# Performance work log

Hardware: AMD Instinct MI355X
Metric: run time of the kernel (lower is better)

The kernel has to match this reference:

```python
import jax, jax.numpy as jnp
import numpy as np
from jax import lax

B, N, D, H, K = 4096, 25, 256, 8, 3  # batch*frames, nodes, d_model, heads, conv kernel


def _layernorm(x, g, b, eps=1e-5):
    mu = jnp.mean(x, axis=-1, keepdims=True)
    var = jnp.var(x, axis=-1, keepdims=True)
    return (x - mu) * lax.rsqrt(var + eps) * g + b


def _conv1d(x_bdn, w):
    # x_bdn: [B, D, N], w: [D_out, D_in, K], padding=K//2 (same as torch Conv1d)
    return lax.conv_general_dilated(x_bdn, w, window_strides=(1,),
                                    padding=[(K // 2, K // 2)],
                                    dimension_numbers=('NCH', 'OIH', 'NCH'))


def setup_inputs() -> dict:
    key = jax.random.key(0)
    ks = jax.random.split(key, 12)
    x = jax.random.normal(ks[0], (B, N, D), dtype=jnp.float32)
    # symmetric adjacency with self-loops (skeleton graph surrogate)
    a = jax.random.bernoulli(ks[1], 0.3, (N, N))
    adj = a | a.T | jnp.eye(N, dtype=bool)
    cs = 1.0 / np.sqrt(D * K)
    wq = jax.random.normal(ks[2], (D, D, K), dtype=jnp.float32) * cs
    wk = jax.random.normal(ks[3], (D, D, K), dtype=jnp.float32) * cs
    wv = jax.random.normal(ks[4], (D, D, K), dtype=jnp.float32) * cs
    gq = jnp.ones((D,), jnp.float32); bq = jnp.zeros((D,), jnp.float32)
    gk = jnp.ones((D,), jnp.float32); bk = jnp.zeros((D,), jnp.float32)
    gv = jnp.ones((D,), jnp.float32); bv = jnp.zeros((D,), jnp.float32)
    rel_table = jax.random.normal(ks[5], (2 * N - 1, H), dtype=jnp.float32) * 0.02
    local_bias = jnp.zeros((H, N, N), jnp.float32)
    wo = jax.random.normal(ks[6], (D, D), dtype=jnp.float32) * (1.0 / np.sqrt(D))
    bo = jnp.zeros((D,), jnp.float32)
    return dict(x=x, adj=adj, wq=wq, wk=wk, wv=wv, gq=gq, bq=bq, gk=gk, bk=bk,
                gv=gv, bv=bv, rel_table=rel_table, local_bias=local_bias, wo=wo, bo=bo)


def reference(x, adj, wq, wk, wv, gq, bq, gk, bk, gv, bv, rel_table, local_bias, wo, bo):
    b, n, d = x.shape
    h = local_bias.shape[0]
    dk = d // h
    xp = x.transpose(0, 2, 1)  # [B, D, N]
    # conv QKV projection over node axis + per-projection LayerNorm + residual
    q = x + _layernorm(_conv1d(xp, wq).transpose(0, 2, 1), gq, bq)
    k = x + _layernorm(_conv1d(xp, wk).transpose(0, 2, 1), gk, bk)
    v = x + _layernorm(_conv1d(xp, wv).transpose(0, 2, 1), gv, bv)
    qh = q.reshape(b, n, h, dk).transpose(0, 2, 1, 3)  # [B, H, N, dk]
    kh = k.reshape(b, n, h, dk).transpose(0, 2, 1, 3)
    vh = v.reshape(b, n, h, dk).transpose(0, 2, 1, 3)
    scores = jnp.einsum('bhnd,bhmd->bhnm', qh, kh) / np.sqrt(dk)
    # relative positional bias over node indices
    coords = jnp.arange(n)
    idx = coords[:, None] - coords[None, :] + n - 1  # [N, N]
    rel = rel_table[idx].transpose(2, 0, 1)  # [H, N, N]
    scores = scores + rel[None] + local_bias[None]
    # adjacency mask (local attention): non-neighbors -> -inf
    scores = jnp.where(adj[None, None], scores, jnp.finfo(scores.dtype).min)
    attn = jax.nn.softmax(scores, axis=-1)
    out = jnp.einsum('bhnm,bhmd->bhnd', attn, vh)  # [B, H, N, dk]
    out = out.transpose(0, 2, 1, 3).reshape(b, n, d)
    return out @ wo.T + bo
```

## Files before the change

kernel.cpp:

```cpp
#include <hip/hip_runtime.h>

#define BB 4096
#define NN 25
#define DD 256
#define HH 8
#define DKH 32
#define MM (BB*NN)

typedef __bf16 bf16;
typedef bf16 bf16x8 __attribute__((ext_vector_type(8)));
typedef bf16 bf16x4 __attribute__((ext_vector_type(4)));
typedef float f32x4 __attribute__((ext_vector_type(4)));
typedef _Float16 h16;
typedef h16 h16x2 __attribute__((ext_vector_type(2)));
typedef h16 h16x4 __attribute__((ext_vector_type(4)));
typedef h16 h16x8 __attribute__((ext_vector_type(8)));

__device__ __forceinline__ void async_load16(const void* g, void* l) {
  __builtin_amdgcn_global_load_lds(
      (const __attribute__((address_space(1))) unsigned int*)g,
      (__attribute__((address_space(3))) unsigned int*)l, 16, 0, 0);
}

#define SCHED_FENCE() __builtin_amdgcn_sched_barrier(0)
#define BARRIER() do { SCHED_FENCE(); __builtin_amdgcn_s_barrier(); SCHED_FENCE(); } while (0)
#define WAIT_LGKM0() do { asm volatile("s_waitcnt lgkmcnt(0)" ::: "memory"); SCHED_FENCE(); } while (0)

__global__ __launch_bounds__(256) void k_prep_xpad(const float* __restrict__ x,
                                                   bf16* __restrict__ xpad) {
  int idx = (blockIdx.x * 256 + threadIdx.x) * 8;
  const int total = BB * 27 * 256;
  if (idx >= total) return;
  int b = idx / (27 * 256);
  int rem = idx - b * 27 * 256;
  int j = rem >> 8;
  int d = rem & 255;
  bf16x8 o;
  if (j >= 1 && j <= 25) {
    const float* src = x + ((b * 25 + (j - 1)) * 256 + d);
    #pragma unroll
    for (int t = 0; t < 8; ++t) o[t] = (bf16)src[t];
  } else {
    #pragma unroll
    for (int t = 0; t < 8; ++t) o[t] = (bf16)0.0f;
  }
  *(bf16x8*)(xpad + idx) = o;
}

__global__ __launch_bounds__(256) void k_prep_misc(
    const float* __restrict__ wq, const float* __restrict__ wk, const float* __restrict__ wv,
    const float* __restrict__ rel, const float* __restrict__ lb, const float* __restrict__ wo,
    const void* __restrict__ adj_raw,
    bf16* __restrict__ Wt, bf16* __restrict__ woB, float* __restrict__ mb) {
  const int NWT = 768 * 768;
  const int NWO = 256 * 256;
  const int NMB = HH * NN * 32;
  const int total = NWT + NWO + NMB;
  for (int i = blockIdx.x * blockDim.x + threadIdx.x; i < total; i += gridDim.x * blockDim.x) {
    if (i < NWT) {
      int j = i / 768, kk = i - j * 768;
      int proj = j >> 8, jo = j & 255;
      int tap = kk >> 8, di = kk & 255;
      const float* w = (proj == 0) ? wq : ((proj == 1) ? wk : wv);
      Wt[i] = (bf16)w[(jo * 256 + di) * 3 + tap];
    } else if (i < NWT + NWO) {
      int t = i - NWT;
      woB[t] = (bf16)wo[t];
    } else {
      int t = i - NWT - NWO;
      int pair = t >> 5;
      int m = t & 31;
      int h = pair / 25, ii = pair - h * 25;
      float v = -1e30f;
      if (m < 25) {
        const unsigned char* bytes = (const unsigned char*)adj_raw;
        bool u8 = false;
        for (int s = 0; s < 625; ++s) {
          if ((s & 3) && bytes[s]) { u8 = true; break; }
        }
        int amask = u8 ? (bytes[ii * 25 + m] ? 1 : 0)
                       : (((const int*)adj_raw)[ii * 25 + m] ? 1 : 0);
        if (amask)
          v = rel[(ii - m + 24) * HH + h] + lb[h * 625 + ii * 25 + m];
      }
      mb[t] = v;
    }
  }
}

__global__ __launch_bounds__(512, 2) void k_qkv_gemm8(const bf16* __restrict__ xpad,
                                                      const bf16* __restrict__ Wt,
                                                      bf16* __restrict__ conv) {
  __shared__ bf16 Ab[2][256 * 64];
  __shared__ bf16 Bb[2][256 * 64];

  const int L = blockIdx.x;
  const int sw = (L & 7) * 150 + (L >> 3);
  const int n0 = (sw % 3) * 256;
  const int m0 = (sw / 3) * 256;

  const int tid = threadIdx.x;
  const int lane = tid & 63, wave = tid >> 6;
  const int t16 = lane & 15, quad = lane >> 4;
  const int wr = wave >> 2, wc = wave & 3;

  const int srow = tid >> 3;
  const int sc = ((tid & 7) << 4) ^ ((srow & 7) << 4);
  int aOff[4], bOff[4];
  #pragma unroll
  for (int q = 0; q < 4; ++q) {
    int row = q * 64 + srow;
    int gm = m0 + row;
    int b = gm / 25;
    int n = gm - b * 25;
    aOff[q] = (b * 27 + n) * 512 + sc;
    bOff[q] = (n0 + row) * 1536 + sc;
  }

  const int axr = (t16 & 7) << 3;
  int aoffs[2], boffs[2];
  #pragma unroll
  for (int kk = 0; kk < 2; ++kk) {
    aoffs[kk] = (wr * 128 + t16) * 64 + ((kk * 32 + quad * 8) ^ axr);
    boffs[kk] = (wc * 64 + t16) * 64 + ((kk * 32 + quad * 8) ^ axr);
  }

  f32x4 acc[8][4];
  #pragma unroll
  for (int i = 0; i < 8; ++i)
    #pragma unroll
    for (int j = 0; j < 4; ++j) acc[i][j] = (f32x4){0.f, 0.f, 0.f, 0.f};

  #pragma unroll
  for (int tt = 0; tt < 2; ++tt) {
    char* lb = (char*)&Bb[tt][0] + wave * 1024;
    char* la = (char*)&Ab[tt][0] + wave * 1024;
    #pragma unroll
    for (int q = 0; q < 4; ++q)
      async_load16((const char*)Wt + bOff[q] + tt * 128, lb + q * 8192);
    #pragma unroll
    for (int q = 0; q < 4; ++q)
      async_load16((const char*)xpad + aOff[q] + tt * 128, la + q * 8192);
  }
  asm volatile("s_waitcnt vmcnt(8)" ::: "memory");
  SCHED_FENCE();
  BARRIER();

  for (int u = 0; u < 12; ++u) {
    const int buf = u & 1;
    const bf16* Ac = &Ab[buf][0];
    const bf16* Bc = &Bb[buf][0];
    const int st = u + 2;

    bf16x8 aF[8], bF[8];

    #pragma unroll
    for (int i = 0; i < 4; ++i)
      #pragma unroll
      for (int kk = 0; kk < 2; ++kk)
        aF[i * 2 + kk] = *(const bf16x8*)(Ac + aoffs[kk] + i * 1024);
    #pragma unroll
    for (int j = 0; j < 2; ++j)
      #pragma unroll
      for (int kk = 0; kk < 2; ++kk)
        bF[j * 2 + kk] = *(const bf16x8*)(Bc + boffs[kk] + j * 1024);
    BARRIER();
    WAIT_LGKM0();
    __builtin_amdgcn_s_setprio(1);
    #pragma unroll
    for (int i = 0; i < 4; ++i)
      #pragma unroll
      for (int j = 0; j < 2; ++j)
        #pragma unroll
        for (int kk = 0; kk < 2; ++kk)
          acc[i][j] = __builtin_amdgcn_mfma_f32_16x16x32_bf16(
              aF[i * 2 + kk], bF[j * 2 + kk], acc[i][j], 0, 0, 0);
    __builtin_amdgcn_s_setprio(0);
    BARRIER();

    #pragma unroll
    for (int j = 0; j < 2; ++j)
      #pragma unroll
      for (int kk = 0; kk < 2; ++kk)
        bF[4 + j * 2 + kk] = *(const bf16x8*)(Bc + boffs[kk] + (2 + j) * 1024);
    BARRIER();
    WAIT_LGKM0();
    __builtin_amdgcn_s_setprio(1);
    #pragma unroll
    for (int i = 0; i < 4; ++i)
      #pragma unroll
      for (int j = 0; j < 2; ++j)
        #pragma unroll
        for (int kk = 0; kk < 2; ++kk)
          acc[i][2 + j] = __builtin_amdgcn_mfma_f32_16x16x32_bf16(
              aF[i * 2 + kk], bF[4 + j * 2 + kk], acc[i][2 + j], 0, 0, 0);
    __builtin_amdgcn_s_setprio(0);
    BARRIER();

    #pragma unroll
    for (int i = 0; i < 4; ++i)
      #pragma unroll
      for (int kk = 0; kk < 2; ++kk)
        aF[i * 2 + kk] = *(const bf16x8*)(Ac + aoffs[kk] + (4 + i) * 1024);
    if (st < 12) {
      char* lb = (char*)&Bb[buf][0] + wave * 1024;
      #pragma unroll
      for (int q = 0; q < 4; ++q)
        async_load16((const char*)Wt + bOff[q] + st * 128, lb + q * 8192);
    }
    BARRIER();
    WAIT_LGKM0();
    __builtin_amdgcn_s_setprio(1);
    #pragma unroll
    for (int i = 0; i < 4; ++i)
      #pragma unroll
      for (int j = 0; j < 2; ++j)
        #pragma unroll
        for (int kk = 0; kk < 2; ++kk)
          acc[4 + i][j] = __builtin_amdgcn_mfma_f32_16x16x32_bf16(
              aF[i * 2 + kk], bF[j * 2 + kk], acc[4 + i][j], 0, 0, 0);
    __builtin_amdgcn_s_setprio(0);
    BARRIER();

    if (st < 12) {
      char* la = (char*)&Ab[buf][0] + wave * 1024;
      const int ka = (st >> 2) * 512 + (st & 3) * 128;
      #pragma unroll
      for (int q = 0; q < 4; ++q)
        async_load16((const char*)xpad + aOff[q] + ka, la + q * 8192);
    }
    BARRIER();
    __builtin_amdgcn_s_setprio(1);
    #pragma unroll
    for (int i = 0; i < 4; ++i)
      #pragma unroll
      for (int j = 0; j < 2; ++j)
        #pragma unroll
        for (int kk = 0; kk < 2; ++kk)
          acc[4 + i][2 + j] = __builtin_amdgcn_mfma_f32_16x16x32_bf16(
              aF[i * 2 + kk], bF[4 + j * 2 + kk], acc[4 + i][2 + j], 0, 0, 0);
    __builtin_amdgcn_s_setprio(0);
    if (u < 10) {
      asm volatile("s_waitcnt vmcnt(8)" ::: "memory");
    } else if (u == 10) {
      asm volatile("s_waitcnt vmcnt(0)" ::: "memory");
    }
    SCHED_FENCE();
    if (u < 11) BARRIER();
  }

  #pragma unroll
  for (int i = 0; i < 8; ++i)
    #pragma unroll
    for (int j = 0; j < 4; ++j) {
      const int col = n0 + wc * 64 + j * 16 + t16;
      #pragma unroll
      for (int r = 0; r < 4; ++r) {
        const int rowm = m0 + wr * 128 + i * 16 + quad * 4 + r;
        conv[(size_t)rowm * 768 + col] = (bf16)acc[i][j][r];
      }
    }
}

__global__ __launch_bounds__(256, 4) void k_attn3(
    const bf16* __restrict__ conv, const float* __restrict__ x,
    const float* __restrict__ gq, const float* __restrict__ bq,
    const float* __restrict__ gk, const float* __restrict__ bk,
    const float* __restrict__ gv, const float* __restrict__ bv,
    const float* __restrict__ mb, bf16* __restrict__ attnout) {
  __shared__ bf16 Cs[19456];
  const int b = blockIdx.x;
  const int tid = threadIdx.x;
  const int wave = tid >> 6, lane = tid & 63;

  const char* slab = (const char*)(conv + (size_t)b * 19200);
  for (int c = wave; c < 38; c += 4)
    async_load16(slab + c * 1024 + lane * 16, (char*)Cs + c * 1024);
  asm volatile("s_waitcnt vmcnt(0)" ::: "memory");
  __syncthreads();

  for (int rowi = wave; rowi < 75; rowi += 4) {
    int n = rowi / 3;
    int p = rowi - n * 3;
    const int off = n * 768 + p * 256 + lane * 4;
    bf16x4 cv = *(const bf16x4*)(Cs + off);
    float v0 = (float)cv[0], v1 = (float)cv[1], v2 = (float)cv[2], v3 = (float)cv[3];
    float s = v0 + v1 + v2 + v3;
    float ss = v0 * v0 + v1 * v1 + v2 * v2 + v3 * v3;
    #pragma unroll
    for (int o = 32; o; o >>= 1) {
      s += __shfl_xor(s, o);
      ss += __shfl_xor(ss, o);
    }
    float mu = s * (1.0f / 256.0f);
    float var = ss * (1.0f / 256.0f) - mu * mu;
    float rs = rsqrtf(var + 1e-5f);
    const float* gsel = (p == 0) ? gq : ((p == 1) ? gk : gv);
    const float* bsel = (p == 0) ? bq : ((p == 1) ? bk : bv);
    const int dbase = lane * 4;
    f32x4 gg = *(const f32x4*)(gsel + dbase);
    f32x4 b2 = *(const f32x4*)(bsel + dbase);
    f32x4 xv = *(const f32x4*)(x + ((size_t)(b * 25 + n)) * 256 + dbase);
    h16x4 o;
    o[0] = (h16)((v0 - mu) * rs * gg[0] + b2[0] + xv[0]);
    o[1] = (h16)((v1 - mu) * rs * gg[1] + b2[1] + xv[1]);
    o[2] = (h16)((v2 - mu) * rs * gg[2] + b2[2] + xv[2]);
    o[3] = (h16)((v3 - mu) * rs * gg[3] + b2[3] + xv[3]);
    *(h16x4*)((h16*)Cs + off) = o;
  }
  __syncthreads();

  const h16* Ch = (const h16*)Cs;
  if (tid < HH * NN) {
    const int h = tid / 25;
    const int i = tid - h * 25;

    h16x2 qv[16];
    const h16x2* qp = (const h16x2*)(Ch + i * 768 + h * 32);
    #pragma unroll
    for (int c = 0; c < 16; ++c) qv[c] = qp[c];

    float mrow[28];
    const float* mbp = mb + (h * 25 + i) * 32;
    #pragma unroll
    for (int c = 0; c < 7; ++c) *(f32x4*)(mrow + c * 4) = *(const f32x4*)(mbp + c * 4);

    const float scale = 0.17677669529663687f;
    float sc[25];
    #pragma unroll
    for (int m = 0; m < 25; ++m) {
      const h16x2* kr = (const h16x2*)(Ch + m * 768 + 256 + h * 32);
      float d = 0.f;
      #pragma unroll
      for (int c = 0; c < 16; ++c)
        d = __builtin_amdgcn_fdot2(qv[c], kr[c], d, false);
      sc[m] = d * scale + mrow[m];
    }

    float mx = sc[0];
    #pragma unroll
    for (int m = 1; m < 25; ++m) mx = fmaxf(mx, sc[m]);
    float sum = 0.f;
    #pragma unroll
    for (int m = 0; m < 25; ++m) { sc[m] = __expf(sc[m] - mx); sum += sc[m]; }
    const float inv = 1.0f / sum;

    h16x2 acc[16];
    #pragma unroll
    for (int j = 0; j < 16; ++j) acc[j] = (h16x2){(h16)0.f, (h16)0.f};
    #pragma unroll
    for (int m = 0; m < 25; ++m) {
      h16 w = (h16)(sc[m] * inv);
      h16x2 wp = {w, w};
      const h16x2* vr = (const h16x2*)(Ch + m * 768 + 512 + h * 32);
      #pragma unroll
      for (int j = 0; j < 16; ++j)
        acc[j] = wp * vr[j] + acc[j];
    }

    bf16* dst = attnout + ((size_t)b * 25 + i) * 256 + h * 32;
    #pragma unroll
    for (int c = 0; c < 4; ++c) {
      bf16x8 o;
      #pragma unroll
      for (int j = 0; j < 4; ++j) {
        o[2 * j]     = (bf16)(float)acc[c * 4 + j][0];
        o[2 * j + 1] = (bf16)(float)acc[c * 4 + j][1];
      }
      *(bf16x8*)(dst + c * 8) = o;
    }
  }
}

__global__ __launch_bounds__(256) void k_outproj(const bf16* __restrict__ attn,
                                                 const bf16* __restrict__ woB,
                                                 const float* __restrict__ bo,
                                                 float* __restrict__ out) {
  __shared__ bf16 As[128 * 32];
  __shared__ bf16 Bs[128 * 32];
  const int L = blockIdx.x;
  const int X = L & 7;
  const int t = L >> 3;
  const int n0 = (t & 1) * 128;
  const int m0 = (X + 8 * (t >> 1)) * 128;
  const int tid = threadIdx.x;
  const int wave = tid >> 6, lane = tid & 63;
  const int quad = lane >> 4, t16 = lane & 15;
  const int wr = wave >> 1, wc = wave & 1;

  f32x4 acc[4][4];
  #pragma unroll
  for (int i = 0; i < 4; ++i)
    #pragma unroll
    for (int j = 0; j < 4; ++j) acc[i][j] = (f32x4){0.f, 0.f, 0.f, 0.f};

  const bf16* baseA[2];
  const bf16* baseB[2];
  #pragma unroll
  for (int r = 0; r < 2; ++r) {
    int c = r * 256 + wave * 64 + lane;
    int row = c >> 2, sub = c & 3;
    baseA[r] = attn + (m0 + row) * 256 + sub * 8;
    baseB[r] = woB + (n0 + row) * 256 + sub * 8;
  }

  for (int ks = 0; ks < 256; ks += 32) {
    #pragma unroll
    for (int r = 0; r < 2; ++r)
      async_load16(baseA[r] + ks, As + (r * 256 + wave * 64) * 8);
    #pragma unroll
    for (int r = 0; r < 2; ++r)
      async_load16(baseB[r] + ks, Bs + (r * 256 + wave * 64) * 8);
    asm volatile("s_waitcnt vmcnt(0)" ::: "memory");
    __syncthreads();

    bf16x8 af[4], bfr[4];
    #pragma unroll
    for (int i = 0; i < 4; ++i)
      af[i] = *(const bf16x8*)(As + (wr * 64 + i * 16 + t16) * 32 + quad * 8);
    #pragma unroll
    for (int j = 0; j < 4; ++j)
      bfr[j] = *(const bf16x8*)(Bs + (wc * 64 + j * 16 + t16) * 32 + quad * 8);
    #pragma unroll
    for (int i = 0; i < 4; ++i)
      #pragma unroll
      for (int j = 0; j < 4; ++j)
        acc[i][j] = __builtin_amdgcn_mfma_f32_16x16x32_bf16(af[i], bfr[j], acc[i][j], 0, 0, 0);
    __syncthreads();
  }

  #pragma unroll
  for (int j = 0; j < 4; ++j) {
    int col = n0 + wc * 64 + j * 16 + t16;
    float bb = bo[col];
    #pragma unroll
    for (int i = 0; i < 4; ++i)
      #pragma unroll
      for (int r = 0; r < 4; ++r) {
        int rowm = m0 + wr * 64 + i * 16 + quad * 4 + r;
        out[rowm * 256 + col] = acc[i][j][r] + bb;
      }
  }
}

extern "C" void kernel_launch(void* const* d_in, const int* in_sizes, int n_in,
                              void* d_out, int out_size, void* d_ws, size_t ws_size,
                              hipStream_t stream) {
  (void)in_sizes; (void)n_in; (void)out_size; (void)ws_size;
  const float* x  = (const float*)d_in[0];
  const void*  adj = d_in[1];
  const float* wq = (const float*)d_in[2];
  const float* wk = (const float*)d_in[3];
  const float* wv = (const float*)d_in[4];
  const float* gq = (const float*)d_in[5];
  const float* bq = (const float*)d_in[6];
  const float* gk = (const float*)d_in[7];
  const float* bk = (const float*)d_in[8];
  const float* gv = (const float*)d_in[9];
  const float* bv = (const float*)d_in[10];
  const float* rel = (const float*)d_in[11];
  const float* lb = (const float*)d_in[12];
  const float* wo = (const float*)d_in[13];
  const float* bo = (const float*)d_in[14];
  float* out = (float*)d_out;

  char* ws = (char*)d_ws;
  size_t off = 0;
  auto alloc = [&](size_t bytes) -> void* {
    void* p = ws + off;
    off += (bytes + 255) & ~(size_t)255;
    return p;
  };
  bf16* xpad = (bf16*)alloc((size_t)BB * 27 * 256 * 2);
  bf16* conv = (bf16*)alloc((size_t)MM * 768 * 2);
  bf16* attn = (bf16*)alloc((size_t)MM * 256 * 2);
  bf16* Wt   = (bf16*)alloc((size_t)768 * 768 * 2);
  bf16* woB  = (bf16*)alloc((size_t)256 * 256 * 2);
  float* mb  = (float*)alloc((size_t)HH * NN * 32 * 4);

  hipLaunchKernelGGL(k_prep_xpad, dim3(13824), dim3(256), 0, stream, x, xpad);
  hipLaunchKernelGGL(k_prep_misc, dim3(512), dim3(256), 0, stream,
                     wq, wk, wv, rel, lb, wo, adj, Wt, woB, mb);
  hipLaunchKernelGGL(k_qkv_gemm8, dim3(1200), dim3(512), 0, stream, xpad, Wt, conv);
  hipLaunchKernelGGL(k_attn3, dim3(4096), dim3(256), 0, stream,
                     conv, x, gq, bq, gk, bk, gv, bv, mb, attn);
  hipLaunchKernelGGL(k_outproj, dim3(1600), dim3(256), 0, stream, attn, woB, bo, out);
}
```

Measured before the change: 549.4 us.

## Software-pipeline LDS fragment loads across GEMM iterations, dropping most barriers

Restructures the conv-projection GEMM main loop so LDS fragment reads for the next k-step are issued during the current step's MFMAs, with Lo/Hi register fragments held across iterations. It removes most per-phase block barriers and the explicit lgkmcnt(0) waits, leaving one barrier per iteration before the buffers are refilled. The aim is to hide LDS latency and cut barrier stalls. The cost is higher register pressure and a trickier vmcnt/barrier ordering, which could be wrong if the counts are off.

New measurement: 554.9 us. Within noise of the previous version (+1.0%).

```diff
diff --git a/kernel.cpp b/kernel.cpp
--- a/kernel.cpp
+++ b/kernel.cpp
@@ -24,7 +24,6 @@
 
 #define SCHED_FENCE() __builtin_amdgcn_sched_barrier(0)
 #define BARRIER() do { SCHED_FENCE(); __builtin_amdgcn_s_barrier(); SCHED_FENCE(); } while (0)
-#define WAIT_LGKM0() do { asm volatile("s_waitcnt lgkmcnt(0)" ::: "memory"); SCHED_FENCE(); } while (0)
 
 __global__ __launch_bounds__(256) void k_prep_xpad(const float* __restrict__ x,
                                                    bf16* __restrict__ xpad) {
@@ -131,41 +130,57 @@
     #pragma unroll
     for (int j = 0; j < 4; ++j) acc[i][j] = (f32x4){0.f, 0.f, 0.f, 0.f};
 
-  #pragma unroll
-  for (int tt = 0; tt < 2; ++tt) {
-    char* lb = (char*)&Bb[tt][0] + wave * 1024;
-    char* la = (char*)&Ab[tt][0] + wave * 1024;
-    #pragma unroll
-    for (int q = 0; q < 4; ++q)
-      async_load16((const char*)Wt + bOff[q] + tt * 128, lb + q * 8192);
-    #pragma unroll
-    for (int q = 0; q < 4; ++q)
-      async_load16((const char*)xpad + aOff[q] + tt * 128, la + q * 8192);
-  }
+  #define ST_B(bufi, tt) do {                                              \
+    char* lb_ = (char*)&Bb[bufi][0] + wave * 1024;                         \
+    _Pragma("unroll")                                                      \
+    for (int q_ = 0; q_ < 4; ++q_)                                         \
+      async_load16((const char*)Wt + bOff[q_] + (tt) * 128, lb_ + q_ * 8192); \
+  } while (0)
+  #define ST_A(bufi, tt) do {                                              \
+    char* la_ = (char*)&Ab[bufi][0] + wave * 1024;                         \
+    const int ka_ = ((tt) >> 2) * 512 + ((tt) & 3) * 128;                  \
+    _Pragma("unroll")                                                      \
+    for (int q_ = 0; q_ < 4; ++q_)                                         \
+      async_load16((const char*)xpad + aOff[q_] + ka_, la_ + q_ * 8192);   \
+  } while (0)
+
+  ST_B(0, 0); ST_A(0, 0);
+  ST_B(1, 1); ST_A(1, 1);
   asm volatile("s_waitcnt vmcnt(8)" ::: "memory");
   SCHED_FENCE();
   BARRIER();
+
+  bf16x8 aLo[8], aHi[8], bLo[4], bHi[4];
+  {
+    const bf16* Ac = &Ab[0][0];
+    const bf16* Bc = &Bb[0][0];
+    #pragma unroll
+    for (int i = 0; i < 4; ++i)
+      #pragma unroll
+      for (int kk = 0; kk < 2; ++kk)
+        aLo[i * 2 + kk] = *(const bf16x8*)(Ac + aoffs[kk] + i * 1024);
+    #pragma unroll
+    for (int j = 0; j < 2; ++j)
+      #pragma unroll
+      for (int kk = 0; kk < 2; ++kk)
+        bLo[j * 2 + kk] = *(const bf16x8*)(Bc + boffs[kk] + j * 1024);
+  }
+  SCHED_FENCE();
 
   for (int u = 0; u < 12; ++u) {
     const int buf = u & 1;
     const bf16* Ac = &Ab[buf][0];
     const bf16* Bc = &Bb[buf][0];
+    const bf16* Ac2 = &Ab[buf ^ 1][0];
+    const bf16* Bc2 = &Bb[buf ^ 1][0];
     const int st = u + 2;
 
-    bf16x8 aF[8], bF[8];
-
-    #pragma unroll
-    for (int i = 0; i < 4; ++i)
+    #pragma unroll
+    for (int j = 0; j < 2; ++j)
       #pragma unroll
       for (int kk = 0; kk < 2; ++kk)
-        aF[i * 2 + kk] = *(const bf16x8*)(Ac + aoffs[kk] + i * 1024);
-    #pragma unroll
-    for (int j = 0; j < 2; ++j)
-      #pragma unroll
-      for (int kk = 0; kk < 2; ++kk)
-        bF[j * 2 + kk] = *(const bf16x8*)(Bc + boffs[kk] + j * 1024);
-    BARRIER();
-    WAIT_LGKM0();
+        bHi[j * 2 + kk] = *(const bf16x8*)(Bc + boffs[kk] + (2 + j) * 1024);
+    SCHED_FENCE();
     __builtin_amdgcn_s_setprio(1);
     #pragma unroll
     for (int i = 0; i < 4; ++i)
@@ -174,17 +189,16 @@
         #pragma unroll
         for (int kk = 0; kk < 2; ++kk)
           acc[i][j] = __builtin_amdgcn_mfma_f32_16x16x32_bf16(
-              aF[i * 2 + kk], bF[j * 2 + kk], acc[i][j], 0, 0, 0);
+              aLo[i * 2 + kk], bLo[j * 2 + kk], acc[i][j], 0, 0, 0);
     __builtin_amdgcn_s_setprio(0);
-    BARRIER();
-
-    #pragma unroll
-    for (int j = 0; j < 2; ++j)
+    SCHED_FENCE();
+
+    #pragma unroll
+    for (int i = 0; i < 4; ++i)
       #pragma unroll
       for (int kk = 0; kk < 2; ++kk)
-        bF[4 + j * 2 + kk] = *(const bf16x8*)(Bc + boffs[kk] + (2 + j) * 1024);
-    BARRIER();
-    WAIT_LGKM0();
+        aHi[i * 2 + kk] = *(const bf16x8*)(Ac + aoffs[kk] + (4 + i) * 1024);
+    SCHED_FENCE();
     __builtin_amdgcn_s_setprio(1);
     #pragma unroll
     for (int i = 0; i < 4; ++i)
@@ -193,23 +207,13 @@
         #pragma unroll
         for (int kk = 0; kk < 2; ++kk)
           acc[i][2 + j] = __builtin_amdgcn_mfma_f32_16x16x32_bf16(
-              aF[i * 2 + kk], bF[4 + j * 2 + kk], acc[i][2 + j], 0, 0, 0);
+              aLo[i * 2 + kk], bHi[j * 2 + kk], acc[i][2 + j], 0, 0, 0);
     __builtin_amdgcn_s_setprio(0);
+    SCHED_FENCE();
+
     BARRIER();
-
-    #pragma unroll
-    for (int i = 0; i < 4; ++i)
-      #pragma unroll
-      for (int kk = 0; kk < 2; ++kk)
-        aF[i * 2 + kk] = *(const bf16x8*)(Ac + aoffs[kk] + (4 + i) * 1024);
-    if (st < 12) {
-      char* lb = (char*)&Bb[buf][0] + wave * 1024;
-      #pragma unroll
-      for (int q = 0; q < 4; ++q)
-        async_load16((const char*)Wt + bOff[q] + st * 128, lb + q * 8192);
-    }
-    BARRIER();
-    WAIT_LGKM0();
+    if (st < 12) ST_B(buf, st);
+    SCHED_FENCE();
     __builtin_amdgcn_s_setprio(1);
     #pragma unroll
     for (int i = 0; i < 4; ++i)
@@ -218,18 +222,31 @@
         #pragma unroll
         for (int kk = 0; kk < 2; ++kk)
           acc[4 + i][j] = __builtin_amdgcn_mfma_f32_16x16x32_bf16(
-              aF[i * 2 + kk], bF[j * 2 + kk], acc[4 + i][j], 0, 0, 0);
+              aHi[i * 2 + kk], bLo[j * 2 + kk], acc[4 + i][j], 0, 0, 0);
     __builtin_amdgcn_s_setprio(0);
-    BARRIER();
-
-    if (st < 12) {
-      char* la = (char*)&Ab[buf][0] + wave * 1024;
-      const int ka = (st >> 2) * 512 + (st & 3) * 128;
-      #pragma unroll
-      for (int q = 0; q < 4; ++q)
-        async_load16((const char*)xpad + aOff[q] + ka, la + q * 8192);
-    }
-    BARRIER();
+    SCHED_FENCE();
+
+    if (u < 11) {
+      if (u < 10) {
+        asm volatile("s_waitcnt vmcnt(4)" ::: "memory");
+      } else {
+        asm volatile("s_waitcnt vmcnt(0)" ::: "memory");
+      }
+      SCHED_FENCE();
+      BARRIER();
+      if (st < 12) ST_A(buf, st);
+      #pragma unroll
+      for (int i = 0; i < 4; ++i)
+        #pragma unroll
+        for (int kk = 0; kk < 2; ++kk)
+          aLo[i * 2 + kk] = *(const bf16x8*)(Ac2 + aoffs[kk] + i * 1024);
+      #pragma unroll
+      for (int j = 0; j < 2; ++j)
+        #pragma unroll
+        for (int kk = 0; kk < 2; ++kk)
+          bLo[j * 2 + kk] = *(const bf16x8*)(Bc2 + boffs[kk] + j * 1024);
+      SCHED_FENCE();
+    }
     __builtin_amdgcn_s_setprio(1);
     #pragma unroll
     for (int i = 0; i < 4; ++i)
@@ -238,16 +255,12 @@
         #pragma unroll
         for (int kk = 0; kk < 2; ++kk)
           acc[4 + i][2 + j] = __builtin_amdgcn_mfma_f32_16x16x32_bf16(
-              aF[i * 2 + kk], bF[4 + j * 2 + kk], acc[4 + i][2 + j], 0, 0, 0);
+              aHi[i * 2 + kk], bHi[j * 2 + kk], acc[4 + i][2 + j], 0, 0, 0);
     __builtin_amdgcn_s_setprio(0);
-    if (u < 10) {
-      asm volatile("s_waitcnt vmcnt(8)" ::: "memory");
-    } else if (u == 10) {
-      asm volatile("s_waitcnt vmcnt(0)" ::: "memory");
-    }
-    SCHED_FENCE();
-    if (u < 11) BARRIER();
-  }
+    SCHED_FENCE();
+  }
+  #undef ST_A
+  #undef ST_B
 
   #pragma unroll
   for (int i = 0; i < 8; ++i)
```
